# Optimization experiments

Measured on AMD Instinct MI355X. Metric: run time of the kernel, lower is better.

## Reference

```python
import jax, jax.numpy as jnp
import numpy as np

EPS = 1e-8  # torch CosineSimilarity default eps


def setup_inputs() -> dict:
    key = jax.random.key(0)
    k_emb, k_idx, k_w1, k_w2 = jax.random.split(key, 4)
    N, H, E = 50000, 128, 800000
    emb = jax.random.normal(k_emb, (N, H), dtype=jnp.float32)
    edge_index = jax.random.randint(k_idx, (2, E), 0, N, dtype=jnp.int64)
    # xavier_uniform for square H x H: limit = sqrt(6 / (H + H))
    lim = float(np.sqrt(6.0 / (H + H)))
    W1 = jax.random.uniform(k_w1, (H, H), dtype=jnp.float32, minval=-lim, maxval=lim)
    W2 = jax.random.uniform(k_w2, (H, H), dtype=jnp.float32, minval=-lim, maxval=lim)
    b1 = jnp.zeros((H,), dtype=jnp.float32)
    b2 = jnp.zeros((H,), dtype=jnp.float32)
    return {"emb": emb, "edge_index": edge_index, "W1": W1, "b1": b1, "W2": W2, "b2": b2}


def reference(emb, edge_index, W1, b1, W2, b2):
    col, row = edge_index[0], edge_index[1]

    def mlp(x):  # Linear -> (Dropout: identity at eval) -> ELU -> Linear
        h = jax.nn.elu(x @ W1.T + b1)
        return h @ W2.T + b2

    f1 = mlp(emb[col])  # [E, H]
    f2 = mlp(emb[row])  # [E, H]
    n1 = jnp.maximum(jnp.sqrt(jnp.sum(f1 * f1, axis=1)), EPS)
    n2 = jnp.maximum(jnp.sqrt(jnp.sum(f2 * f2, axis=1)), EPS)
    return jnp.sum(f1 * f2, axis=1) / (n1 * n2)  # [E]
```

## Files before the change

kernel.cpp:

```cpp
#include <hip/hip_runtime.h>
#include <math.h>

#define H 128
#define MROWS 64
#define XS 136

typedef __attribute__((ext_vector_type(8))) short short8;
typedef __attribute__((ext_vector_type(4))) float floatx4;

__device__ __forceinline__ unsigned short f2bf(float f) {
    unsigned u = __float_as_uint(f);
    return (unsigned short)((u + 0x7FFFu + ((u >> 16) & 1u)) >> 16);
}

__global__ void prep_weights(const float* __restrict__ W1,
                             const float* __restrict__ W2,
                             unsigned short* __restrict__ Wbf) {
    int i = blockIdx.x * 256 + threadIdx.x;
    if (i < 16384)       Wbf[i] = f2bf(W1[i]);
    else if (i < 32768)  Wbf[i] = f2bf(W2[i - 16384]);
}

__global__ __launch_bounds__(256, 2) void mlp_mfma(
    const float* __restrict__ emb, const unsigned short* __restrict__ Wbf,
    const float* __restrict__ b1, const float* __restrict__ b2,
    signed char* __restrict__ qtab, float* __restrict__ scl, int N)
{
    __shared__ unsigned short Wl[H * XS];
    __shared__ char dbuf[2 * MROWS * XS * 2];
    __shared__ float invn_s[MROWS];
    __shared__ float amax_s[MROWS];

    unsigned short* xs = (unsigned short*)dbuf;
    unsigned short* hs = xs + MROWS * XS;
    float*          gs = (float*)dbuf;

    const int tid   = threadIdx.x;
    const int wave  = tid >> 6, lane = tid & 63;
    const int quad  = lane >> 4, l15 = lane & 15;
    const int node0 = blockIdx.x * MROWS;

    {
        const float4* src = (const float4*)Wbf;
        #pragma unroll
        for (int i = 0; i < 8; ++i) {
            int cc = i * 256 + tid;
            int row = cc >> 4, c = cc & 15;
            *(float4*)(Wl + row * XS + c * 8) = src[cc];
        }
    }
    #pragma unroll
    for (int i = 0; i < 8; ++i) {
        int flat = i * 1024 + tid * 4;
        int rowl = flat >> 7, col = flat & 127;
        float4 v = make_float4(0.f, 0.f, 0.f, 0.f);
        if (node0 + rowl < N)
            v = *(const float4*)(emb + (size_t)(node0 + rowl) * H + col);
        ushort4 b;
        b.x = f2bf(v.x); b.y = f2bf(v.y); b.z = f2bf(v.z); b.w = f2bf(v.w);
        *(ushort4*)(xs + rowl * XS + col) = b;
    }
    __syncthreads();

    short8 afr[4];
    const int mrow = wave * 16 + l15;

    #pragma unroll
    for (int ks = 0; ks < 4; ++ks)
        afr[ks] = *(const short8*)(xs + mrow * XS + ks * 32 + quad * 8);
    #pragma unroll
    for (int nt = 0; nt < 8; ++nt) {
        floatx4 acc = {0.f, 0.f, 0.f, 0.f};
        #pragma unroll
        for (int ks = 0; ks < 4; ++ks) {
            short8 bfr = *(const short8*)(Wl + (nt * 16 + l15) * XS + ks * 32 + quad * 8);
            acc = __builtin_amdgcn_mfma_f32_16x16x32_bf16(afr[ks], bfr, acc, 0, 0, 0);
        }
        const int col = nt * 16 + l15;
        const float bb = b1[col];
        #pragma unroll
        for (int r = 0; r < 4; ++r) {
            float v = acc[r] + bb;
            v = v > 0.f ? v : (__expf(v) - 1.f);
            hs[(wave * 16 + quad * 4 + r) * XS + col] = f2bf(v);
        }
    }
    __syncthreads();

    {
        const float4* src = (const float4*)(Wbf + 16384);
        #pragma unroll
        for (int i = 0; i < 8; ++i) {
            int cc = i * 256 + tid;
            int row = cc >> 4, c = cc & 15;
            *(float4*)(Wl + row * XS + c * 8) = src[cc];
        }
    }
    __syncthreads();

    #pragma unroll
    for (int ks = 0; ks < 4; ++ks)
        afr[ks] = *(const short8*)(hs + mrow * XS + ks * 32 + quad * 8);
    __syncthreads();

    float sq[4] = {0.f, 0.f, 0.f, 0.f};
    float am[4] = {0.f, 0.f, 0.f, 0.f};
    #pragma unroll
    for (int nt = 0; nt < 8; ++nt) {
        floatx4 acc = {0.f, 0.f, 0.f, 0.f};
        #pragma unroll
        for (int ks = 0; ks < 4; ++ks) {
            short8 bfr = *(const short8*)(Wl + (nt * 16 + l15) * XS + ks * 32 + quad * 8);
            acc = __builtin_amdgcn_mfma_f32_16x16x32_bf16(afr[ks], bfr, acc, 0, 0, 0);
        }
        const int col = nt * 16 + l15;
        const float bb = b2[col];
        #pragma unroll
        for (int r = 0; r < 4; ++r) {
            float v = acc[r] + bb;
            gs[(wave * 16 + quad * 4 + r) * H + col] = v;
            sq[r] += v * v;
            am[r] = fmaxf(am[r], fabsf(v));
        }
    }
    #pragma unroll
    for (int r = 0; r < 4; ++r) {
        float s = sq[r], a = am[r];
        #pragma unroll
        for (int m = 8; m; m >>= 1) {
            s += __shfl_xor(s, m);
            a = fmaxf(a, __shfl_xor(a, m));
        }
        if (l15 == 0) {
            const int row = wave * 16 + quad * 4 + r;
            float nn = sqrtf(s);
            if (nn < 1e-8f) nn = 1e-8f;
            invn_s[row] = 1.f / nn;
            amax_s[row] = fmaxf(a, 1e-20f);
        }
    }
    __syncthreads();

    if (tid < MROWS && node0 + tid < N)
        scl[node0 + tid] = amax_s[tid] * invn_s[tid] * (1.f / 127.f);

    #pragma unroll
    for (int i = 0; i < 2; ++i) {
        int chunk = i * 256 + tid;
        int row = chunk >> 3, c0 = (chunk & 7) * 16;
        if (node0 + row < N) {
            const float qs = 127.f / amax_s[row];
            unsigned u[4];
            #pragma unroll
            for (int w = 0; w < 4; ++w) {
                unsigned pk = 0;
                #pragma unroll
                for (int j = 0; j < 4; ++j) {
                    float v = gs[row * H + c0 + w * 4 + j] * qs;
                    int q = (int)rintf(v);
                    q = q > 127 ? 127 : (q < -127 ? -127 : q);
                    pk |= ((unsigned)(q & 255)) << (8 * j);
                }
                u[w] = pk;
            }
            *(uint4*)(qtab + (size_t)(node0 + row) * H + c0) =
                make_uint4(u[0], u[1], u[2], u[3]);
        }
    }
}

__device__ __forceinline__ int dot4(unsigned a, unsigned b) {
    int s = 0;
    #pragma unroll
    for (int j = 0; j < 4; ++j)
        s += (int)((signed char)(a >> (8 * j))) * (int)((signed char)(b >> (8 * j)));
    return s;
}

__global__ __launch_bounds__(256) void edge_cos(
    const int* __restrict__ ei, const signed char* __restrict__ qtab,
    const float* __restrict__ scl, float* __restrict__ out, int E)
{
    const int gid = blockIdx.x * 256 + threadIdx.x;
    const int e = gid >> 3, sub = gid & 7;
    if (e >= E) return;

    const int c = ei[e];
    const int r = ei[e + E];

    const uint4 ua = *(const uint4*)(qtab + (size_t)c * H + sub * 16);
    const uint4 ub = *(const uint4*)(qtab + (size_t)r * H + sub * 16);
    int s = dot4(ua.x, ub.x) + dot4(ua.y, ub.y)
          + dot4(ua.z, ub.z) + dot4(ua.w, ub.w);

    #pragma unroll
    for (int m = 4; m; m >>= 1) s += __shfl_xor(s, m);
    if (sub == 0) out[e] = (float)s * scl[c] * scl[r];
}

extern "C" void kernel_launch(void* const* d_in, const int* in_sizes, int n_in,
                              void* d_out, int out_size, void* d_ws, size_t ws_size,
                              hipStream_t stream) {
    const float* emb = (const float*)d_in[0];
    const int*   ei  = (const int*)d_in[1];
    const float* W1  = (const float*)d_in[2];
    const float* b1  = (const float*)d_in[3];
    const float* W2  = (const float*)d_in[4];
    const float* b2  = (const float*)d_in[5];
    float*       out = (float*)d_out;

    const int N = in_sizes[0] / H;
    const int E = in_sizes[1] / 2;

    unsigned short* Wbf  = (unsigned short*)d_ws;
    signed char*    qtab = (signed char*)(Wbf + 32768);
    float*          scl  = (float*)(qtab + (size_t)N * H);

    prep_weights<<<128, 256, 0, stream>>>(W1, W2, Wbf);
    mlp_mfma<<<(N + MROWS - 1) / MROWS, 256, 0, stream>>>(emb, Wbf, b1, b2, qtab, scl, N);
    edge_cos<<<(E * 8 + 255) / 256, 256, 0, stream>>>(ei, qtab, scl, out, E);
}
```

Baseline: 123.5 us.

## Load MLP A-fragments from global directly, shrink LDS, use sdot4 and nontemporal access

```diff
diff --git a/kernel.cpp b/kernel.cpp
--- a/kernel.cpp
+++ b/kernel.cpp
@@ -4,6 +4,7 @@
 #define H 128
 #define MROWS 64
 #define XS 136
+#define GS 132
 
 typedef __attribute__((ext_vector_type(8))) short short8;
 typedef __attribute__((ext_vector_type(4))) float floatx4;
@@ -21,24 +22,36 @@
     else if (i < 32768)  Wbf[i] = f2bf(W2[i - 16384]);
 }
 
-__global__ __launch_bounds__(256, 2) void mlp_mfma(
+__global__ __launch_bounds__(256, 3) void mlp_mfma(
     const float* __restrict__ emb, const unsigned short* __restrict__ Wbf,
     const float* __restrict__ b1, const float* __restrict__ b2,
     signed char* __restrict__ qtab, float* __restrict__ scl, int N)
 {
     __shared__ unsigned short Wl[H * XS];
-    __shared__ char dbuf[2 * MROWS * XS * 2];
-    __shared__ float invn_s[MROWS];
+    __shared__ unsigned short hs[MROWS * XS];
     __shared__ float amax_s[MROWS];
-
-    unsigned short* xs = (unsigned short*)dbuf;
-    unsigned short* hs = xs + MROWS * XS;
-    float*          gs = (float*)dbuf;
+    float* gs = (float*)Wl;
 
     const int tid   = threadIdx.x;
     const int wave  = tid >> 6, lane = tid & 63;
     const int quad  = lane >> 4, l15 = lane & 15;
     const int node0 = blockIdx.x * MROWS;
+    const int mrow_g = node0 + wave * 16 + l15;
+
+    short8 afr[4];
+    #pragma unroll
+    for (int ks = 0; ks < 4; ++ks) {
+        float4 f0 = make_float4(0.f, 0.f, 0.f, 0.f), f1 = f0;
+        if (mrow_g < N) {
+            const float* p = emb + (size_t)mrow_g * H + ks * 32 + quad * 8;
+            f0 = *(const float4*)p;
+            f1 = *(const float4*)(p + 4);
+        }
+        short8 a;
+        a[0] = f2bf(f0.x); a[1] = f2bf(f0.y); a[2] = f2bf(f0.z); a[3] = f2bf(f0.w);
+        a[4] = f2bf(f1.x); a[5] = f2bf(f1.y); a[6] = f2bf(f1.z); a[7] = f2bf(f1.w);
+        afr[ks] = a;
+    }
 
     {
         const float4* src = (const float4*)Wbf;
@@ -49,25 +62,8 @@
             *(float4*)(Wl + row * XS + c * 8) = src[cc];
         }
     }
-    #pragma unroll
-    for (int i = 0; i < 8; ++i) {
-        int flat = i * 1024 + tid * 4;
-        int rowl = flat >> 7, col = flat & 127;
-        float4 v = make_float4(0.f, 0.f, 0.f, 0.f);
-        if (node0 + rowl < N)
-            v = *(const float4*)(emb + (size_t)(node0 + rowl) * H + col);
-        ushort4 b;
-        b.x = f2bf(v.x); b.y = f2bf(v.y); b.z = f2bf(v.z); b.w = f2bf(v.w);
-        *(ushort4*)(xs + rowl * XS + col) = b;
-    }
-    __syncthreads();
-
-    short8 afr[4];
-    const int mrow = wave * 16 + l15;
-
-    #pragma unroll
-    for (int ks = 0; ks < 4; ++ks)
-        afr[ks] = *(const short8*)(xs + mrow * XS + ks * 32 + quad * 8);
+    __syncthreads();
+
     #pragma unroll
     for (int nt = 0; nt < 8; ++nt) {
         floatx4 acc = {0.f, 0.f, 0.f, 0.f};
@@ -96,15 +92,12 @@
             *(float4*)(Wl + row * XS + c * 8) = src[cc];
         }
     }
-    __syncthreads();
-
     #pragma unroll
     for (int ks = 0; ks < 4; ++ks)
-        afr[ks] = *(const short8*)(hs + mrow * XS + ks * 32 + quad * 8);
-    __syncthreads();
-
-    float sq[4] = {0.f, 0.f, 0.f, 0.f};
-    float am[4] = {0.f, 0.f, 0.f, 0.f};
+        afr[ks] = *(const short8*)(hs + (wave * 16 + l15) * XS + ks * 32 + quad * 8);
+    __syncthreads();
+
+    floatx4 acc2[8];
     #pragma unroll
     for (int nt = 0; nt < 8; ++nt) {
         floatx4 acc = {0.f, 0.f, 0.f, 0.f};
@@ -113,36 +106,50 @@
             short8 bfr = *(const short8*)(Wl + (nt * 16 + l15) * XS + ks * 32 + quad * 8);
             acc = __builtin_amdgcn_mfma_f32_16x16x32_bf16(afr[ks], bfr, acc, 0, 0, 0);
         }
-        const int col = nt * 16 + l15;
-        const float bb = b2[col];
+        const float bb = b2[nt * 16 + l15];
+        #pragma unroll
+        for (int r = 0; r < 4; ++r) acc[r] += bb;
+        acc2[nt] = acc;
+    }
+
+    float sq[4] = {0.f, 0.f, 0.f, 0.f};
+    float am[4] = {0.f, 0.f, 0.f, 0.f};
+    #pragma unroll
+    for (int nt = 0; nt < 8; ++nt)
         #pragma unroll
         for (int r = 0; r < 4; ++r) {
-            float v = acc[r] + bb;
-            gs[(wave * 16 + quad * 4 + r) * H + col] = v;
+            float v = acc2[nt][r];
             sq[r] += v * v;
             am[r] = fmaxf(am[r], fabsf(v));
         }
-    }
     #pragma unroll
     for (int r = 0; r < 4; ++r) {
-        float s = sq[r], a = am[r];
         #pragma unroll
         for (int m = 8; m; m >>= 1) {
-            s += __shfl_xor(s, m);
-            a = fmaxf(a, __shfl_xor(a, m));
-        }
+            sq[r] += __shfl_xor(sq[r], m);
+            am[r] = fmaxf(am[r], __shfl_xor(am[r], m));
+        }
+        am[r] = fmaxf(am[r], 1e-20f);
         if (l15 == 0) {
-            const int row = wave * 16 + quad * 4 + r;
-            float nn = sqrtf(s);
-            if (nn < 1e-8f) nn = 1e-8f;
-            invn_s[row] = 1.f / nn;
-            amax_s[row] = fmaxf(a, 1e-20f);
-        }
-    }
-    __syncthreads();
-
-    if (tid < MROWS && node0 + tid < N)
-        scl[node0 + tid] = amax_s[tid] * invn_s[tid] * (1.f / 127.f);
+            const int grow = node0 + wave * 16 + quad * 4 + r;
+            amax_s[wave * 16 + quad * 4 + r] = am[r];
+            if (grow < N) {
+                float nn = sqrtf(sq[r]);
+                if (nn < 1e-8f) nn = 1e-8f;
+                scl[grow] = am[r] / (127.f * nn);
+            }
+        }
+    }
+    __syncthreads();
+
+    #pragma unroll
+    for (int nt = 0; nt < 8; ++nt) {
+        const int col = nt * 16 + l15;
+        #pragma unroll
+        for (int r = 0; r < 4; ++r)
+            gs[(wave * 16 + quad * 4 + r) * GS + col] = acc2[nt][r];
+    }
+    __syncthreads();
 
     #pragma unroll
     for (int i = 0; i < 2; ++i) {
@@ -156,7 +163,7 @@
                 unsigned pk = 0;
                 #pragma unroll
                 for (int j = 0; j < 4; ++j) {
-                    float v = gs[row * H + c0 + w * 4 + j] * qs;
+                    float v = gs[row * GS + c0 + w * 4 + j] * qs;
                     int q = (int)rintf(v);
                     q = q > 127 ? 127 : (q < -127 ? -127 : q);
                     pk |= ((unsigned)(q & 255)) << (8 * j);
@@ -169,12 +176,15 @@
     }
 }
 
-__device__ __forceinline__ int dot4(unsigned a, unsigned b) {
-    int s = 0;
+__device__ __forceinline__ int dot4acc(unsigned a, unsigned b, int s) {
+#if __has_builtin(__builtin_amdgcn_sdot4)
+    return __builtin_amdgcn_sdot4((int)a, (int)b, s, false);
+#else
     #pragma unroll
     for (int j = 0; j < 4; ++j)
         s += (int)((signed char)(a >> (8 * j))) * (int)((signed char)(b >> (8 * j)));
     return s;
+#endif
 }
 
 __global__ __launch_bounds__(256) void edge_cos(
@@ -185,17 +195,23 @@
     const int e = gid >> 3, sub = gid & 7;
     if (e >= E) return;
 
-    const int c = ei[e];
-    const int r = ei[e + E];
+    const int c = __builtin_nontemporal_load(&ei[e]);
+    const int r = __builtin_nontemporal_load(&ei[e + E]);
 
     const uint4 ua = *(const uint4*)(qtab + (size_t)c * H + sub * 16);
     const uint4 ub = *(const uint4*)(qtab + (size_t)r * H + sub * 16);
-    int s = dot4(ua.x, ub.x) + dot4(ua.y, ub.y)
-          + dot4(ua.z, ub.z) + dot4(ua.w, ub.w);
+    int s = 0;
+    s = dot4acc(ua.x, ub.x, s);
+    s = dot4acc(ua.y, ub.y, s);
+    s = dot4acc(ua.z, ub.z, s);
+    s = dot4acc(ua.w, ub.w, s);
 
     #pragma unroll
     for (int m = 4; m; m >>= 1) s += __shfl_xor(s, m);
-    if (sub == 0) out[e] = (float)s * scl[c] * scl[r];
+    if (sub == 0) {
+        float v = (float)s * scl[c] * scl[r];
+        __builtin_nontemporal_store(v, &out[e]);
+    }
 }
 
 extern "C" void kernel_launch(void* const* d_in, const int* in_sizes, int n_in,
@@ -217,6 +233,7 @@
     float*          scl  = (float*)(qtab + (size_t)N * H);
 
     prep_weights<<<128, 256, 0, stream>>>(W1, W2, Wbf);
-    mlp_mfma<<<(N + MROWS - 1) / MROWS, 256, 0, stream>>>(emb, Wbf, b1, b2, qtab, scl, N);
+    mlp_mfma<<<(N + MROWS - 1) / MROWS, 256, 0, stream>>>(
+        emb, Wbf, b1, b2, qtab, scl, N);
     edge_cos<<<(E * 8 + 255) / 256, 256, 0, stream>>>(ei, qtab, scl, out, E);
 }
```

Result: no change. 124.3 us (+0.7%).
